# Performance work log

Measured on AMD Instinct MI355X. Metric: run time of the kernel, lower is better.

## Reference

```python
import jax, jax.numpy as jnp
import numpy as np

UNITS = 1024
IN_DIM = 1024
BATCH = 8192


def setup_inputs() -> dict:
    key = jax.random.key(0)
    ks = jax.random.split(key, 8)
    return {
        "inputs": jax.random.normal(ks[0], (BATCH, IN_DIM), dtype=jnp.float32),
        "c_prev": jax.random.normal(ks[1], (BATCH, UNITS), dtype=jnp.float32),
        "h_prev": jax.random.normal(ks[2], (BATCH, UNITS), dtype=jnp.float32),
        "kernel": jax.random.normal(ks[3], (IN_DIM, 4 * UNITS), dtype=jnp.float32) * 0.02,
        "recurrent_kernel": jax.random.normal(ks[4], (UNITS, 4 * UNITS), dtype=jnp.float32) * 0.02,
        "bias": jnp.zeros((4 * UNITS,), dtype=jnp.float32),
        "peephole_f": jax.random.normal(ks[5], (UNITS,), dtype=jnp.float32) * 0.1,
        "peephole_i": jax.random.normal(ks[6], (UNITS,), dtype=jnp.float32) * 0.1,
        "peephole_o": jax.random.normal(ks[7], (UNITS,), dtype=jnp.float32) * 0.1,
    }


def reference(inputs, c_prev, h_prev, kernel, recurrent_kernel, bias,
              peephole_f, peephole_i, peephole_o):
    # z: [B, 4U] = x @ W + h_prev @ U + b
    z = inputs @ kernel + h_prev @ recurrent_kernel + bias
    z_f, z_i, z_c, z_o = jnp.split(z, 4, axis=1)
    f = jax.nn.sigmoid(z_f + peephole_f * c_prev)
    i = jax.nn.sigmoid(z_i + peephole_i * c_prev)
    c_tilde = jnp.tanh(z_c)
    c = f * c_prev + i * c_tilde
    o = jax.nn.sigmoid(z_o + peephole_o * c)
    h = o * jnp.tanh(c)
    return h, c
```

## Files before the change

kernel.cpp:

```cpp
#include <hip/hip_runtime.h>

typedef unsigned short u16;
typedef __attribute__((ext_vector_type(8))) short bf16x8;
typedef __attribute__((ext_vector_type(4))) float f32x4;

constexpr int BATCH = 8192;
constexpr int UNITS = 1024;
constexpr int K2    = 2048;
constexpr int N4    = 4096;
constexpr int BK    = 64;

__device__ __forceinline__ u16 f2bf(float f) {
  unsigned u = __float_as_uint(f);
  u += 0x7fffu + ((u >> 16) & 1u);
  return (u16)(u >> 16);
}

__device__ __forceinline__ void async_copy16(const void* g, void* l) {
  __builtin_amdgcn_global_load_lds(
      (const __attribute__((address_space(1))) void*)g,
      (__attribute__((address_space(3))) void*)l, 16, 0, 0);
}

__global__ __launch_bounds__(256) void cast_fused_kernel(
    const float* __restrict__ x, const float* __restrict__ h,
    const float* __restrict__ W, const float* __restrict__ U,
    u16* __restrict__ A, u16* __restrict__ B) {
  const int tid = threadIdx.x;
  if (blockIdx.x < 2048) {
    __shared__ float lds[64 * 69];
    const int bid = blockIdx.x;
    const int nb  = bid & 63;
    const int kb  = bid >> 6;
    const int n0  = nb * 64;
    const int k0  = kb * 64;
    const int jn  = n0 >> 10;
    const int q0  = (n0 & 1023) >> 4;
    const float* src = (k0 < UNITS) ? (W + (size_t)k0 * N4)
                                    : (U + (size_t)(k0 - UNITS) * N4);
    {
      const int kk  = tid >> 4;
      const int nn4 = (tid & 15) * 4;
#pragma unroll
      for (int r = 0; r < 4; ++r) {
        const int k = kk + r * 16;
        float4 v = *reinterpret_cast<const float4*>(&src[(size_t)k * N4 + n0 + nn4]);
        lds[k * 69 + nn4 + 0] = v.x;
        lds[k * 69 + nn4 + 1] = v.y;
        lds[k * 69 + nn4 + 2] = v.z;
        lds[k * 69 + nn4 + 3] = v.w;
      }
    }
    __syncthreads();
    {
      const int kk4 = (tid & 15) * 4;
#pragma unroll
      for (int pass = 0; pass < 4; ++pass) {
        const int rr  = (tid >> 4) + pass * 16;
        const int q   = q0 + (rr >> 4);
        const int low = rr & 15;
        const int p   = q * 64 + jn * 16 + low;
        union { ushort4 u4; u16 s[4]; } o;
#pragma unroll
        for (int j = 0; j < 4; ++j) o.s[j] = f2bf(lds[(kk4 + j) * 69 + rr]);
        *reinterpret_cast<ushort4*>(&B[(size_t)p * K2 + k0 + kk4]) = o.u4;
      }
    }
  } else {
    const int t0 = (blockIdx.x - 2048) * 256 + tid;
    const int stride = 4096 * 256;
#pragma unroll
    for (int s = 0; s < 4; ++s) {
      const int g = t0 + s * stride;
      const int idx = g * 4;
      const int b = idx >> 11;
      const int k = idx & 2047;
      const float* src = (k < UNITS) ? (x + (size_t)b * UNITS + k)
                                     : (h + (size_t)b * UNITS + (k - UNITS));
      float4 v = *reinterpret_cast<const float4*>(src);
      union { ushort4 u4; u16 sv[4]; } o;
      o.sv[0] = f2bf(v.x); o.sv[1] = f2bf(v.y);
      o.sv[2] = f2bf(v.z); o.sv[3] = f2bf(v.w);
      *reinterpret_cast<ushort4*>(A + idx) = o.u4;
    }
  }
}

__global__ __launch_bounds__(256, 4) void lstm_gemm_kernel(
    const u16* __restrict__ A, const u16* __restrict__ B,
    const float* __restrict__ bias, const float* __restrict__ c_prev,
    const float* __restrict__ pf, const float* __restrict__ pi,
    const float* __restrict__ po,
    float* __restrict__ out_h, float* __restrict__ out_c) {
  __shared__ u16 As[128 * BK];
  __shared__ u16 Bs[128 * BK];

  const int tid  = threadIdx.x;
  const int lane = tid & 63;
  const int wave = tid >> 6;
  const int quad = lane >> 4;
  const int c    = lane & 15;
  const int m0   = blockIdx.y * 128;
  const int n0   = blockIdx.x * 128;
  const int wm   = (wave >> 1) * 64;
  const int wn   = (wave & 1) * 64;

  const int g8 = ((lane & 7) ^ ((lane >> 3) & 7)) * 8;
  const int r0 = wave * 32 + (lane >> 3);
  const u16* ga = A + (size_t)(m0 + r0) * K2 + g8;
  const u16* gb = B + (size_t)(n0 + r0) * K2 + g8;
  u16* la = &As[(wave * 256 + lane) * 8];
  u16* lb = &Bs[(wave * 256 + lane) * 8];

  f32x4 acc[4][4] = {};

  for (int kt = 0; kt < K2 / BK; ++kt) {
#pragma unroll
    for (int i = 0; i < 4; ++i) {
      async_copy16(ga + (size_t)i * 8 * K2, la + i * 512);
      async_copy16(gb + (size_t)i * 8 * K2, lb + i * 512);
    }
    ga += BK; gb += BK;
    __syncthreads();

#pragma unroll
    for (int ks = 0; ks < 2; ++ks) {
      bf16x8 af[4], bfr[4];
#pragma unroll
      for (int j = 0; j < 4; ++j) {
        const int sl = ((ks * 4 + quad) ^ (c & 7)) * 8;
        af[j]  = *(const bf16x8*)&As[(wm + j * 16 + c) * BK + sl];
        bfr[j] = *(const bf16x8*)&Bs[(wn + j * 16 + c) * BK + sl];
      }
#pragma unroll
      for (int jm = 0; jm < 4; ++jm)
#pragma unroll
        for (int jn = 0; jn < 4; ++jn)
          acc[jm][jn] = __builtin_amdgcn_mfma_f32_16x16x32_bf16(
              af[jm], bfr[jn], acc[jm][jn], 0, 0, 0);
    }
    __syncthreads();
  }

  const int u = ((n0 + wn) >> 2) + c;
  const float bf_ = bias[u];
  const float bi_ = bias[UNITS + u];
  const float bc_ = bias[2 * UNITS + u];
  const float bo_ = bias[3 * UNITS + u];
  const float pfv = pf[u], piv = pi[u], pov = po[u];
  const int mbase = m0 + wm + quad * 4;
#pragma unroll
  for (int jm = 0; jm < 4; ++jm) {
#pragma unroll
    for (int r = 0; r < 4; ++r) {
      const int b = mbase + jm * 16 + r;
      const float cp = c_prev[(size_t)b * UNITS + u];
      const float zf = acc[jm][0][r] + bf_ + pfv * cp;
      const float zi = acc[jm][1][r] + bi_ + piv * cp;
      const float zc = acc[jm][2][r] + bc_;
      const float zo = acc[jm][3][r] + bo_;
      const float fg = 1.f / (1.f + __expf(-zf));
      const float ig = 1.f / (1.f + __expf(-zi));
      const float ct = 1.f - 2.f / (__expf(2.f * zc) + 1.f);
      const float cn = fg * cp + ig * ct;
      const float og = 1.f / (1.f + __expf(-(zo + pov * cn)));
      const float hn = og * (1.f - 2.f / (__expf(2.f * cn) + 1.f));
      out_h[(size_t)b * UNITS + u] = hn;
      out_c[(size_t)b * UNITS + u] = cn;
    }
  }
}

extern "C" void kernel_launch(void* const* d_in, const int* in_sizes, int n_in,
                              void* d_out, int out_size, void* d_ws, size_t ws_size,
                              hipStream_t stream) {
  const float* x      = (const float*)d_in[0];
  const float* c_prev = (const float*)d_in[1];
  const float* h_prev = (const float*)d_in[2];
  const float* W      = (const float*)d_in[3];
  const float* U      = (const float*)d_in[4];
  const float* bias   = (const float*)d_in[5];
  const float* pf     = (const float*)d_in[6];
  const float* pi     = (const float*)d_in[7];
  const float* po     = (const float*)d_in[8];
  float* out_h = (float*)d_out;
  float* out_c = out_h + (size_t)BATCH * UNITS;

  u16* Abf = (u16*)d_ws;
  u16* Bbf = Abf + (size_t)BATCH * K2;

  cast_fused_kernel<<<6144, 256, 0, stream>>>(x, h_prev, W, U, Abf, Bbf);
  lstm_gemm_kernel<<<dim3(N4 / 128, BATCH / 128), 256, 0, stream>>>(
      Abf, Bbf, bias, c_prev, pf, pi, po, out_h, out_c);
}
```

Baseline: 193.8 us.

## Enlarge GEMM tiles to 256x256 with multi-stage pipelined LDS loads

Rewrites the LSTM GEMM kernel to use 256x256 block tiles with 512 threads. It adds a triple-buffered A and double-buffered B LDS pipeline whose async loads are interleaved into four MFMA phases, with explicit waitcnt, barriers and setprio. It also remaps block indices for L2 locality. The aim is to hide global-load latency behind MFMA work and to raise arithmetic intensity per loaded tile. In exchange it uses more LDS (160 KB per block) and more registers, which lowers occupancy, and the hand-tuned synchronization is fragile.

```diff
diff --git a/kernel.cpp b/kernel.cpp
--- a/kernel.cpp
+++ b/kernel.cpp
@@ -9,6 +9,11 @@
 constexpr int K2    = 2048;
 constexpr int N4    = 4096;
 constexpr int BK    = 64;
+constexpr int BM    = 256;
+constexpr int BN    = 256;
+constexpr int NKT   = K2 / BK;
+constexpr int ASZ   = BM * BK;
+constexpr int BSZ   = BN * BK;
 
 __device__ __forceinline__ u16 f2bf(float f) {
   unsigned u = __float_as_uint(f);
@@ -86,60 +91,129 @@
   }
 }
 
-__global__ __launch_bounds__(256, 4) void lstm_gemm_kernel(
+__global__ __launch_bounds__(512, 2) void lstm_gemm_kernel(
     const u16* __restrict__ A, const u16* __restrict__ B,
     const float* __restrict__ bias, const float* __restrict__ c_prev,
     const float* __restrict__ pf, const float* __restrict__ pi,
     const float* __restrict__ po,
     float* __restrict__ out_h, float* __restrict__ out_c) {
-  __shared__ u16 As[128 * BK];
-  __shared__ u16 Bs[128 * BK];
+  __shared__ u16 lds[3 * ASZ + 2 * BSZ];
+  u16* const Asb = lds;
+  u16* const Bsb = lds + 3 * ASZ;
 
   const int tid  = threadIdx.x;
   const int lane = tid & 63;
   const int wave = tid >> 6;
   const int quad = lane >> 4;
   const int c    = lane & 15;
-  const int m0   = blockIdx.y * 128;
-  const int n0   = blockIdx.x * 128;
-  const int wm   = (wave >> 1) * 64;
-  const int wn   = (wave & 1) * 64;
-
-  const int g8 = ((lane & 7) ^ ((lane >> 3) & 7)) * 8;
-  const int r0 = wave * 32 + (lane >> 3);
-  const u16* ga = A + (size_t)(m0 + r0) * K2 + g8;
-  const u16* gb = B + (size_t)(n0 + r0) * K2 + g8;
-  u16* la = &As[(wave * 256 + lane) * 8];
-  u16* lb = &Bs[(wave * 256 + lane) * 8];
-
-  f32x4 acc[4][4] = {};
-
-  for (int kt = 0; kt < K2 / BK; ++kt) {
-#pragma unroll
-    for (int i = 0; i < 4; ++i) {
-      async_copy16(ga + (size_t)i * 8 * K2, la + i * 512);
-      async_copy16(gb + (size_t)i * 8 * K2, lb + i * 512);
-    }
-    ga += BK; gb += BK;
-    __syncthreads();
-
-#pragma unroll
-    for (int ks = 0; ks < 2; ++ks) {
-      bf16x8 af[4], bfr[4];
-#pragma unroll
-      for (int j = 0; j < 4; ++j) {
-        const int sl = ((ks * 4 + quad) ^ (c & 7)) * 8;
-        af[j]  = *(const bf16x8*)&As[(wm + j * 16 + c) * BK + sl];
-        bfr[j] = *(const bf16x8*)&Bs[(wn + j * 16 + c) * BK + sl];
-      }
-#pragma unroll
-      for (int jm = 0; jm < 4; ++jm)
+
+  int lin = blockIdx.y * 16 + blockIdx.x;
+  lin = (lin & 7) * 64 + (lin >> 3);
+  const int m0 = (lin >> 4) * BM;
+  const int n0 = (lin & 15) * BN;
+
+  const int wm = (wave >> 2) * 128;
+  const int wn = (wave & 3) * 64;
+
+  const int g8   = ((tid & 7) ^ ((tid >> 3) & 7)) * 8;
+  const int rowa = tid >> 3;
+  const u16* gA = A + (size_t)(m0 + rowa) * K2 + g8;
+  const u16* gB = B + (size_t)(n0 + rowa) * K2 + g8;
+  const int ldst = tid * 8;
+
+  const int sl0   = (quad ^ (c & 7)) * 8;
+  const int sl1   = ((4 + quad) ^ (c & 7)) * 8;
+  const int aoff0 = (wm + c) * 64 + sl0;
+  const int aoff1 = (wm + c) * 64 + sl1;
+  const int boff0 = (wn + c) * 64 + sl0;
+  const int boff1 = (wn + c) * 64 + sl1;
+
+  f32x4 acc[8][4] = {};
+
+#pragma unroll
+  for (int i = 0; i < 4; ++i)
+    async_copy16(gA + (size_t)i * 64 * K2, &Asb[i * 4096 + ldst]);
+#pragma unroll
+  for (int i = 0; i < 4; ++i)
+    async_copy16(gB + (size_t)i * 64 * K2, &Bsb[i * 4096 + ldst]);
+#pragma unroll
+  for (int i = 0; i < 4; ++i)
+    async_copy16(gA + (size_t)i * 64 * K2 + BK, &Asb[ASZ + i * 4096 + ldst]);
+  asm volatile("s_waitcnt vmcnt(4)" ::: "memory");
+  __builtin_amdgcn_s_barrier();
+  __builtin_amdgcn_sched_barrier(0);
+
+  int curA = 0;
+#pragma unroll 1
+  for (int kt = 0; kt < NKT; ++kt) {
+    const u16* as = &Asb[curA * ASZ];
+    const u16* bs = &Bsb[(kt & 1) * BSZ];
+    const int stgA = (curA == 0) ? 2 : curA - 1;
+    u16* sA = &Asb[stgA * ASZ];
+    u16* sB = &Bsb[((kt + 1) & 1) * BSZ];
+    const bool doB = (kt < NKT - 1);
+    const bool doA = (kt < NKT - 2);
+    const size_t okB = (size_t)(kt + 1) * BK;
+    const size_t okA = (size_t)(kt + 2) * BK;
+
+    bf16x8 bfr[2][4];
+#pragma unroll
+    for (int ph = 0; ph < 4; ++ph) {
+      if (ph == 0 && doB) {
+        async_copy16(gB + okB,                     sB + ldst);
+        async_copy16(gB + okB + (size_t)64 * K2,   sB + 4096 + ldst);
+      }
+      if (ph == 1 && doB) {
+        async_copy16(gB + okB + (size_t)128 * K2,  sB + 8192 + ldst);
+        async_copy16(gB + okB + (size_t)192 * K2,  sB + 12288 + ldst);
+      }
+      if (ph == 2 && doA) {
+        async_copy16(gA + okA,                     sA + ldst);
+        async_copy16(gA + okA + (size_t)64 * K2,   sA + 4096 + ldst);
+      }
+      if (ph == 3 && doA) {
+        async_copy16(gA + okA + (size_t)128 * K2,  sA + 8192 + ldst);
+        async_copy16(gA + okA + (size_t)192 * K2,  sA + 12288 + ldst);
+      }
+      if (ph == 0) {
+#pragma unroll
+        for (int jn = 0; jn < 4; ++jn) {
+          bfr[0][jn] = *(const bf16x8*)(bs + boff0 + jn * 1024);
+          bfr[1][jn] = *(const bf16x8*)(bs + boff1 + jn * 1024);
+        }
+      }
+      bf16x8 af0[2], af1[2];
+#pragma unroll
+      for (int jm = 0; jm < 2; ++jm) {
+        af0[jm] = *(const bf16x8*)(as + aoff0 + (2 * ph + jm) * 1024);
+        af1[jm] = *(const bf16x8*)(as + aoff1 + (2 * ph + jm) * 1024);
+      }
+      if (ph == 3) {
+        if (kt < NKT - 2)       asm volatile("s_waitcnt vmcnt(4)" ::: "memory");
+        else if (kt == NKT - 2) asm volatile("s_waitcnt vmcnt(0)" ::: "memory");
+      }
+      __builtin_amdgcn_s_barrier();
+      __builtin_amdgcn_sched_barrier(0);
+      __builtin_amdgcn_s_setprio(1);
+#pragma unroll
+      for (int jm = 0; jm < 2; ++jm)
 #pragma unroll
         for (int jn = 0; jn < 4; ++jn)
-          acc[jm][jn] = __builtin_amdgcn_mfma_f32_16x16x32_bf16(
-              af[jm], bfr[jn], acc[jm][jn], 0, 0, 0);
-    }
-    __syncthreads();
+          acc[2 * ph + jm][jn] = __builtin_amdgcn_mfma_f32_16x16x32_bf16(
+              af0[jm], bfr[0][jn], acc[2 * ph + jm][jn], 0, 0, 0);
+#pragma unroll
+      for (int jm = 0; jm < 2; ++jm)
+#pragma unroll
+        for (int jn = 0; jn < 4; ++jn)
+          acc[2 * ph + jm][jn] = __builtin_amdgcn_mfma_f32_16x16x32_bf16(
+              af1[jm], bfr[1][jn], acc[2 * ph + jm][jn], 0, 0, 0);
+      __builtin_amdgcn_s_setprio(0);
+      if (!(ph == 3 && kt == NKT - 1)) {
+        __builtin_amdgcn_s_barrier();
+        __builtin_amdgcn_sched_barrier(0);
+      }
+    }
+    curA = (curA == 2) ? 0 : curA + 1;
   }
 
   const int u = ((n0 + wn) >> 2) + c;
@@ -150,7 +224,7 @@
   const float pfv = pf[u], piv = pi[u], pov = po[u];
   const int mbase = m0 + wm + quad * 4;
 #pragma unroll
-  for (int jm = 0; jm < 4; ++jm) {
+  for (int jm = 0; jm < 8; ++jm) {
 #pragma unroll
     for (int r = 0; r < 4; ++r) {
       const int b = mbase + jm * 16 + r;
@@ -190,6 +264,6 @@
   u16* Bbf = Abf + (size_t)BATCH * K2;
 
   cast_fused_kernel<<<6144, 256, 0, stream>>>(x, h_prev, W, U, Abf, Bbf);
-  lstm_gemm_kernel<<<dim3(N4 / 128, BATCH / 128), 256, 0, stream>>>(
+  lstm_gemm_kernel<<<dim3(N4 / BN, BATCH / BM), 512, 0, stream>>>(
       Abf, Bbf, bias, c_prev, pf, pi, po, out_h, out_c);
 }
```

Result: faster. 161.4 us (-16.7%).
